# Kernel tuning notes

Hardware: AMD Instinct MI355X
Metric: run time of the kernel (lower is better)

Reference implementation:

```python
import jax, jax.numpy as jnp
import numpy as np

N = 20000      # nodes
E = 320000     # directed edges (self-loops added inside reference)
DIN = 128      # input_dim
HID = 64       # hidden_dim
H = 4          # num_heads
B = 16         # graphs in batch
OUT = 1        # output_dim
NEG_SLOPE = 0.2


def setup_inputs() -> dict:
    key = jax.random.key(0)
    ks = jax.random.split(key, 20)
    p = lambda k, shape: (jax.random.normal(k, shape, jnp.float32) * 0.05)
    x = jax.random.normal(ks[0], (N, DIN), jnp.float32)
    edge_index = jax.random.randint(ks[1], (2, E), 0, N, dtype=jnp.int64)
    batch = jnp.sort(jax.random.randint(ks[2], (N,), 0, B, dtype=jnp.int64))
    return {
        "x": x, "edge_index": edge_index, "batch": batch,
        # gat1: DIN -> (H, HID), concat
        "W1": p(ks[3], (DIN, H * HID)), "as1": p(ks[4], (H, HID)), "ad1": p(ks[5], (H, HID)), "b1": jnp.zeros((H * HID,), jnp.float32),
        # gat2: H*HID -> (H, HID), concat
        "W2": p(ks[6], (H * HID, H * HID)), "as2": p(ks[7], (H, HID)), "ad2": p(ks[8], (H, HID)), "b2": jnp.zeros((H * HID,), jnp.float32),
        # gat_out: H*HID -> (1, HID), mean (concat=False)
        "W3": p(ks[9], (H * HID, HID)), "as3": p(ks[10], (1, HID)), "ad3": p(ks[11], (1, HID)), "b3": jnp.zeros((HID,), jnp.float32),
        "wp": p(ks[12], (HID, 1)), "bp": jnp.zeros((1,), jnp.float32),
        "wr": p(ks[13], (HID, OUT)), "br": jnp.zeros((OUT,), jnp.float32),
    }


def _gat_layer(x, W, a_src, a_dst, bias, src, dst, heads, concat):
    n = x.shape[0]
    h = (x @ W).reshape(n, heads, -1)                      # [N,H,C]
    e_src = (h * a_src).sum(-1)                            # [N,H]
    e_dst = (h * a_dst).sum(-1)                            # [N,H]
    e = jax.nn.leaky_relu(e_src[src] + e_dst[dst], NEG_SLOPE)  # [Etot,H]
    # segment softmax over destination node (self-loops guarantee non-empty)
    m = jax.ops.segment_max(e, dst, num_segments=n)
    e = jnp.exp(e - m[dst])
    den = jax.ops.segment_sum(e, dst, num_segments=n)
    alpha = e / den[dst]                                   # [Etot,H]
    out = jax.ops.segment_sum(h[src] * alpha[..., None], dst, num_segments=n)  # [N,H,C]
    out = out.reshape(n, -1) if concat else out.mean(axis=1)
    return out + bias


def reference(x, edge_index, batch, W1, as1, ad1, b1, W2, as2, ad2, b2,
              W3, as3, ad3, b3, wp, bp, wr, br):
    n = x.shape[0]
    loops = jnp.arange(n, dtype=edge_index.dtype)
    src = jnp.concatenate([edge_index[0], loops])
    dst = jnp.concatenate([edge_index[1], loops])

    h = jax.nn.elu(_gat_layer(x, W1, as1, ad1, b1, src, dst, H, True))
    h = jax.nn.elu(_gat_layer(h, W2, as2, ad2, b2, src, dst, H, True))
    h = jax.nn.elu(_gat_layer(h, W3, as3, ad3, b3, src, dst, 1, False))  # [N,HID]

    attn = jax.nn.sigmoid(h @ wp + bp)                     # [N,1]
    hw = h * attn                                          # [N,HID]
    sums = jax.ops.segment_sum(hw, batch, num_segments=B)  # [B,HID]
    counts = jax.ops.segment_sum(jnp.ones((n,), hw.dtype), batch, num_segments=B)
    pooled = sums / jnp.maximum(counts, 1.0)[:, None]
    return pooled @ wr + br                                # [B,OUT]
```

## Files before the change

kernel.cpp:

```cpp
#include <hip/hip_runtime.h>


typedef unsigned short u16;
typedef __attribute__((ext_vector_type(8))) short bf16x8;
typedef __attribute__((ext_vector_type(4))) float f32x4;

__device__ __forceinline__ u16 bf16rn(float x) {
    unsigned u = __float_as_uint(x);
    u += 0x7FFFu + ((u >> 16) & 1u);
    return (u16)(u >> 16);
}
__device__ __forceinline__ float bf16f(u16 h) {
    return __uint_as_float(((unsigned)h) << 16);
}

__device__ __forceinline__ void gload16(const u16* g, u16* l) {
    __builtin_amdgcn_global_load_lds(
        (const __attribute__((address_space(1))) unsigned int*)g,
        (__attribute__((address_space(3))) unsigned int*)l, 16, 0, 0);
}

__global__ void edge_hist_k(const int* __restrict__ ei, int E, int n, int* __restrict__ deg) {
    int i = blockIdx.x * blockDim.x + threadIdx.x;
    if (i >= E + n) return;
    int dst = (i < E) ? ei[E + i] : (i - E);
    atomicAdd(&deg[dst], 1);
}

__global__ __launch_bounds__(1024) void scan_excl_k(const int* __restrict__ deg, int* __restrict__ rowptr,
                                                    int* __restrict__ cursor, int n) {
    __shared__ int part[1024];
    int tid = threadIdx.x;
    int chunk = (n + 1023) / 1024;
    int lo = tid * chunk;
    int hi = lo + chunk;
    if (lo > n) lo = n;
    if (hi > n) hi = n;
    int s = 0;
    for (int i = lo; i < hi; ++i) s += deg[i];
    part[tid] = s;
    __syncthreads();
    for (int off = 1; off < 1024; off <<= 1) {
        int v = (tid >= off) ? part[tid - off] : 0;
        __syncthreads();
        part[tid] += v;
        __syncthreads();
    }
    int run = (tid == 0) ? 0 : part[tid - 1];
    for (int i = lo; i < hi; ++i) {
        rowptr[i] = run;
        cursor[i] = run;
        run += deg[i];
    }
    if (tid == 1023) rowptr[n] = run;
}

__global__ void edge_scatter_k(const int* __restrict__ ei, int E, int n,
                               int* __restrict__ cursor, int* __restrict__ srcs) {
    int i = blockIdx.x * blockDim.x + threadIdx.x;
    if (i >= E + n) return;
    int src, dst;
    if (i < E) { src = ei[i]; dst = ei[E + i]; }
    else       { src = i - E; dst = src; }
    int pos = atomicAdd(&cursor[dst], 1);
    srcs[pos] = src;
}

__global__ void split_bf16_k(const float* __restrict__ in, u16* __restrict__ hi,
                             u16* __restrict__ lo, int n4) {
    int i = blockIdx.x * 256 + threadIdx.x;
    if (i >= n4) return;
    float4 v = reinterpret_cast<const float4*>(in)[i];
    u16 hx = bf16rn(v.x), hy = bf16rn(v.y), hz = bf16rn(v.z), hw = bf16rn(v.w);
    ushort4 H = make_ushort4(hx, hy, hz, hw);
    ushort4 L = make_ushort4(bf16rn(v.x - bf16f(hx)), bf16rn(v.y - bf16f(hy)),
                             bf16rn(v.z - bf16f(hz)), bf16rn(v.w - bf16f(hw)));
    reinterpret_cast<ushort4*>(hi)[i] = H;
    reinterpret_cast<ushort4*>(lo)[i] = L;
}

__global__ void splitT_bf16_k(const float* __restrict__ W, u16* __restrict__ thi,
                              u16* __restrict__ tlo, int K, int Nn) {
    int idx = blockIdx.x * 256 + threadIdx.x;
    if (idx >= K * Nn) return;
    int k = idx / Nn, nn = idx - k * Nn;
    float v = W[idx];
    u16 h = bf16rn(v);
    u16 l = bf16rn(v - bf16f(h));
    thi[(size_t)nn * K + k] = h;
    tlo[(size_t)nn * K + k] = l;
}

template <int NF>
__global__ __launch_bounds__(256) void gemm_lds_k(
        const u16* __restrict__ Ahi, const u16* __restrict__ Alo,
        const u16* __restrict__ Bthi, const u16* __restrict__ Btlo,
        float* __restrict__ C, int M, int Nn, int K) {
    __shared__ u16 Ah[2][4][64 * 8];
    __shared__ u16 Al[2][4][64 * 8];
    const int mb = (M + 63) >> 6;
    const int mi = blockIdx.x % mb;
    const int ni = blockIdx.x / mb;
    const int m0 = mi * 64;
    const int n0 = ni * (NF * 64);
    const int wv = threadIdx.x >> 6;
    const int lane = threadIdx.x & 63;
    const int rr = lane & 15;
    const int kg = lane >> 4;

    int srow = m0 + lane; if (srow > M - 1) srow = M - 1;
    const u16* sh = Ahi + (size_t)srow * K + wv * 8;
    const u16* sl = Alo + (size_t)srow * K + wv * 8;

    const u16* pbh[NF];
    const u16* pbl[NF];
#pragma unroll
    for (int nf = 0; nf < NF; ++nf) {
        int col = n0 + (wv * NF + nf) * 16 + rr;
        pbh[nf] = Bthi + (size_t)col * K + kg * 8;
        pbl[nf] = Btlo + (size_t)col * K + kg * 8;
    }

    f32x4 acc[4][NF];
#pragma unroll
    for (int mf = 0; mf < 4; ++mf)
#pragma unroll
        for (int nf = 0; nf < NF; ++nf) acc[mf][nf] = (f32x4){0.f, 0.f, 0.f, 0.f};

    bf16x8 bhc[NF], blc[NF], bhn[NF], bln[NF];
#pragma unroll
    for (int nf = 0; nf < NF; ++nf) {
        bhc[nf] = *reinterpret_cast<const bf16x8*>(pbh[nf]);
        blc[nf] = *reinterpret_cast<const bf16x8*>(pbl[nf]);
    }
    gload16(sh, &Ah[0][wv][0]);
    gload16(sl, &Al[0][wv][0]);
    __syncthreads();

    const int NT = K >> 5;
    for (int t = 0; t < NT; ++t) {
        const int cur = t & 1;
        if (t + 1 < NT) {
            const int kc = (t + 1) << 5;
#pragma unroll
            for (int nf = 0; nf < NF; ++nf) {
                bhn[nf] = *reinterpret_cast<const bf16x8*>(pbh[nf] + kc);
                bln[nf] = *reinterpret_cast<const bf16x8*>(pbl[nf] + kc);
            }
            gload16(sh + kc, &Ah[cur ^ 1][wv][0]);
            gload16(sl + kc, &Al[cur ^ 1][wv][0]);
        }
        bf16x8 ah[4], al[4];
#pragma unroll
        for (int mf = 0; mf < 4; ++mf) {
            ah[mf] = *reinterpret_cast<const bf16x8*>(&Ah[cur][kg][(mf * 16 + rr) * 8]);
            al[mf] = *reinterpret_cast<const bf16x8*>(&Al[cur][kg][(mf * 16 + rr) * 8]);
        }
#pragma unroll
        for (int mf = 0; mf < 4; ++mf)
#pragma unroll
            for (int nf = 0; nf < NF; ++nf) {
                acc[mf][nf] = __builtin_amdgcn_mfma_f32_16x16x32_bf16(ah[mf], bhc[nf], acc[mf][nf], 0, 0, 0);
                acc[mf][nf] = __builtin_amdgcn_mfma_f32_16x16x32_bf16(ah[mf], blc[nf], acc[mf][nf], 0, 0, 0);
                acc[mf][nf] = __builtin_amdgcn_mfma_f32_16x16x32_bf16(al[mf], bhc[nf], acc[mf][nf], 0, 0, 0);
            }
#pragma unroll
        for (int nf = 0; nf < NF; ++nf) { bhc[nf] = bhn[nf]; blc[nf] = bln[nf]; }
        __syncthreads();
    }

#pragma unroll
    for (int mf = 0; mf < 4; ++mf)
#pragma unroll
        for (int nf = 0; nf < NF; ++nf)
#pragma unroll
            for (int rg = 0; rg < 4; ++rg) {
                int row = m0 + mf * 16 + kg * 4 + rg;
                if (row < M)
                    C[(size_t)row * Nn + n0 + (wv * NF + nf) * 16 + rr] = acc[mf][nf][rg];
            }
}

__global__ void attn_scores4_k(const float* __restrict__ hin, const float* __restrict__ a_src,
                               const float* __restrict__ a_dst, float* __restrict__ esrc,
                               float* __restrict__ edst, int n) {
    int node = blockIdx.x * 4 + (threadIdx.x >> 6);
    int lane = threadIdx.x & 63;
    if (node >= n) return;
    float4 hv  = *reinterpret_cast<const float4*>(&hin[(size_t)node * 256 + lane * 4]);
    float4 asv = *reinterpret_cast<const float4*>(&a_src[lane * 4]);
    float4 adv = *reinterpret_cast<const float4*>(&a_dst[lane * 4]);
    float vs = hv.x * asv.x + hv.y * asv.y + hv.z * asv.z + hv.w * asv.w;
    float vd = hv.x * adv.x + hv.y * adv.y + hv.z * adv.z + hv.w * adv.w;
#pragma unroll
    for (int off = 8; off; off >>= 1) {
        vs += __shfl_xor(vs, off);
        vd += __shfl_xor(vd, off);
    }
    if ((lane & 15) == 0) {
        int h = lane >> 4;
        esrc[node * 4 + h] = vs;
        edst[node * 4 + h] = vd;
    }
}

__global__ void attn_scores1_k(const float* __restrict__ hin, const float* __restrict__ a_src,
                               const float* __restrict__ a_dst, float* __restrict__ esrc,
                               float* __restrict__ edst, int n) {
    int node = blockIdx.x * 4 + (threadIdx.x >> 6);
    int lane = threadIdx.x & 63;
    if (node >= n) return;
    float hv = hin[(size_t)node * 64 + lane];
    float vs = hv * a_src[lane];
    float vd = hv * a_dst[lane];
#pragma unroll
    for (int off = 32; off; off >>= 1) {
        vs += __shfl_xor(vs, off);
        vd += __shfl_xor(vd, off);
    }
    if (lane == 0) { esrc[node] = vs; edst[node] = vd; }
}

__global__ __launch_bounds__(256) void gat_aggregate4_k(
        const float* __restrict__ hin, const float* __restrict__ esrc,
        const float* __restrict__ edst, const int* __restrict__ rowptr,
        const int* __restrict__ srcs, const float* __restrict__ bias,
        u16* __restrict__ ghi, u16* __restrict__ glo, int n) {
    int d = blockIdx.x * 4 + (threadIdx.x >> 6);
    int lane = threadIdx.x & 63;
    if (d >= n) return;
    int hh = lane >> 4;
    float ed = edst[d * 4 + hh];
    int lo = rowptr[d], hi = rowptr[d + 1];
    float4 acc = make_float4(0.f, 0.f, 0.f, 0.f);
    float den = 0.f;
    for (int base = lo; base < hi; base += 64) {
        int cnt = min(64, hi - base);
        int sv = (lane < cnt) ? srcs[base + lane] : 0;
        int s0 = __shfl(sv, 0);
        float es0 = esrc[s0 * 4 + hh];
        float4 h0 = *reinterpret_cast<const float4*>(&hin[(size_t)s0 * 256 + lane * 4]);
        float es1 = 0.f;
        float4 h1 = h0;
        if (cnt > 1) {
            int s1 = __shfl(sv, 1);
            es1 = esrc[s1 * 4 + hh];
            h1 = *reinterpret_cast<const float4*>(&hin[(size_t)s1 * 256 + lane * 4]);
        }
        for (int j = 0; j < cnt; ++j) {
            float es = es0;
            float4 hv = h0;
            es0 = es1; h0 = h1;
            if (j + 2 < cnt) {
                int s2 = __shfl(sv, j + 2);
                es1 = esrc[s2 * 4 + hh];
                h1 = *reinterpret_cast<const float4*>(&hin[(size_t)s2 * 256 + lane * 4]);
            }
            float e = es + ed;
            e = (e >= 0.f) ? e : 0.2f * e;
            float w = __expf(e);
            den += w;
            acc.x = fmaf(w, hv.x, acc.x);
            acc.y = fmaf(w, hv.y, acc.y);
            acc.z = fmaf(w, hv.z, acc.z);
            acc.w = fmaf(w, hv.w, acc.w);
        }
    }
    float inv = 1.f / den;
    float4 bv = *reinterpret_cast<const float4*>(&bias[lane * 4]);
    float4 o;
    o.x = acc.x * inv + bv.x;
    o.y = acc.y * inv + bv.y;
    o.z = acc.z * inv + bv.z;
    o.w = acc.w * inv + bv.w;
    o.x = (o.x > 0.f) ? o.x : expm1f(o.x);
    o.y = (o.y > 0.f) ? o.y : expm1f(o.y);
    o.z = (o.z > 0.f) ? o.z : expm1f(o.z);
    o.w = (o.w > 0.f) ? o.w : expm1f(o.w);
    u16 hx = bf16rn(o.x), hy = bf16rn(o.y), hz = bf16rn(o.z), hw = bf16rn(o.w);
    ushort4 H = make_ushort4(hx, hy, hz, hw);
    ushort4 L = make_ushort4(bf16rn(o.x - bf16f(hx)), bf16rn(o.y - bf16f(hy)),
                             bf16rn(o.z - bf16f(hz)), bf16rn(o.w - bf16f(hw)));
    *reinterpret_cast<ushort4*>(&ghi[(size_t)d * 256 + lane * 4]) = H;
    *reinterpret_cast<ushort4*>(&glo[(size_t)d * 256 + lane * 4]) = L;
}

__global__ __launch_bounds__(256) void gat_aggregate1_attn_k(
        const float* __restrict__ hin, const float* __restrict__ esrc,
        const float* __restrict__ edst, const int* __restrict__ rowptr,
        const int* __restrict__ srcs, const float* __restrict__ bias,
        const float* __restrict__ wp, const float* __restrict__ bp,
        float* __restrict__ gout, float* __restrict__ attn, int n) {
    int d = blockIdx.x * 4 + (threadIdx.x >> 6);
    int lane = threadIdx.x & 63;
    if (d >= n) return;
    float ed = edst[d];
    int lo = rowptr[d], hi = rowptr[d + 1];
    float den = 0.f, acc = 0.f;
    for (int base = lo; base < hi; base += 64) {
        int cnt = min(64, hi - base);
        int sv = (lane < cnt) ? srcs[base + lane] : 0;
        int s0 = __shfl(sv, 0);
        float es_nxt = esrc[s0];
        float h_nxt = hin[(size_t)s0 * 64 + lane];
        for (int j = 0; j < cnt; ++j) {
            float es = es_nxt;
            float hv = h_nxt;
            if (j + 1 < cnt) {
                int s1 = __shfl(sv, j + 1);
                es_nxt = esrc[s1];
                h_nxt = hin[(size_t)s1 * 64 + lane];
            }
            float e = es + ed;
            e = (e >= 0.f) ? e : 0.2f * e;
            float w = __expf(e);
            den += w;
            acc = fmaf(w, hv, acc);
        }
    }
    float o = acc / den + bias[lane];
    o = (o > 0.f) ? o : expm1f(o);
    gout[(size_t)d * 64 + lane] = o;
    float v = o * wp[lane];
#pragma unroll
    for (int off = 32; off; off >>= 1) v += __shfl_xor(v, off);
    if (lane == 0) attn[d] = 1.f / (1.f + __expf(-(v + bp[0])));
}

__global__ void pool_partial_k(const float* __restrict__ g3, const float* __restrict__ attn,
                               const int* __restrict__ batch, int n, float* __restrict__ sums) {
    int wid = blockIdx.x * (blockDim.x >> 6) + (threadIdx.x >> 6);
    int lane = threadIdx.x & 63;
    int nwaves = gridDim.x * (blockDim.x >> 6);
    int per = (n + nwaves - 1) / nwaves;
    int i0 = wid * per;
    int i1 = i0 + per;
    if (i1 > n) i1 = n;
    if (i0 >= i1) return;
    int cur = batch[i0];
    float acc = 0.f;
    for (int i = i0; i < i1; ++i) {
        int b = batch[i];
        if (b != cur) {
            atomicAdd(&sums[cur * 64 + lane], acc);
            acc = 0.f;
            cur = b;
        }
        acc += g3[(size_t)i * 64 + lane] * attn[i];
    }
    atomicAdd(&sums[cur * 64 + lane], acc);
}

__global__ void regress_k(const float* __restrict__ sums, const int* __restrict__ batch, int n,
                          const float* __restrict__ wr, const float* __restrict__ br,
                          float* __restrict__ out, int B) {
    int b = threadIdx.x >> 6;
    int lane = threadIdx.x & 63;
    if (b >= B) return;
    int lo = 0, hi = n;
    while (lo < hi) { int mid = (lo + hi) >> 1; if (batch[mid] < b) lo = mid + 1; else hi = mid; }
    int seg_lo = lo;
    lo = 0; hi = n;
    while (lo < hi) { int mid = (lo + hi) >> 1; if (batch[mid] < b + 1) lo = mid + 1; else hi = mid; }
    float cnt = (float)(lo - seg_lo);
    if (cnt < 1.f) cnt = 1.f;
    float v = (sums[b * 64 + lane] / cnt) * wr[lane];
#pragma unroll
    for (int off = 32; off; off >>= 1) v += __shfl_xor(v, off);
    if (lane == 0) out[b] = v + br[0];
}

extern "C" void kernel_launch(void* const* d_in, const int* in_sizes, int n_in,
                              void* d_out, int out_size, void* d_ws, size_t ws_size,
                              hipStream_t stream) {
    const float* x   = (const float*)d_in[0];
    const int*   ei  = (const int*)d_in[1];
    const int*   bat = (const int*)d_in[2];
    const float* W1  = (const float*)d_in[3];
    const float* as1 = (const float*)d_in[4];
    const float* ad1 = (const float*)d_in[5];
    const float* b1  = (const float*)d_in[6];
    const float* W2  = (const float*)d_in[7];
    const float* as2 = (const float*)d_in[8];
    const float* ad2 = (const float*)d_in[9];
    const float* b2  = (const float*)d_in[10];
    const float* W3  = (const float*)d_in[11];
    const float* as3 = (const float*)d_in[12];
    const float* ad3 = (const float*)d_in[13];
    const float* b3  = (const float*)d_in[14];
    const float* wp  = (const float*)d_in[15];
    const float* bp  = (const float*)d_in[16];
    const float* wr  = (const float*)d_in[17];
    const float* br  = (const float*)d_in[18];
    float* out = (float*)d_out;

    const int N    = in_sizes[2];
    const int E    = in_sizes[1] / 2;
    const int DIN  = in_sizes[0] / N;
    const int Etot = E + N;
    const int Bc   = out_size;

    char* ws = (char*)d_ws;
    size_t off = 0;
    auto alloc = [&](size_t bytes) {
        void* p = ws + off;
        off = (off + bytes + 255) & ~(size_t)255;
        return p;
    };
    int*   deg    = (int*)alloc((size_t)N * 4);
    int*   rowptr = (int*)alloc((size_t)(N + 1) * 4);
    int*   cursor = (int*)alloc((size_t)N * 4);
    int*   srcs   = (int*)alloc((size_t)Etot * 4);
    float* bufA   = (float*)alloc((size_t)N * 256 * 4);
    u16*   Ahi    = (u16*)alloc((size_t)N * 256 * 2);
    u16*   Alo    = (u16*)alloc((size_t)N * 256 * 2);
    float* h3     = (float*)alloc((size_t)N * 64 * 4);
    float* g3     = (float*)alloc((size_t)N * 64 * 4);
    float* esrc   = (float*)alloc((size_t)N * 4 * 4);
    float* edst   = (float*)alloc((size_t)N * 4 * 4);
    float* attn   = (float*)alloc((size_t)N * 4);
    float* sums   = (float*)alloc((size_t)Bc * 64 * 4);
    u16*   w1hi   = (u16*)alloc((size_t)256 * DIN * 2);
    u16*   w1lo   = (u16*)alloc((size_t)256 * DIN * 2);
    u16*   w2hi   = (u16*)alloc((size_t)256 * 256 * 2);
    u16*   w2lo   = (u16*)alloc((size_t)256 * 256 * 2);
    u16*   w3hi   = (u16*)alloc((size_t)64 * 256 * 2);
    u16*   w3lo   = (u16*)alloc((size_t)64 * 256 * 2);
    (void)ws_size;

    hipMemsetAsync(deg, 0, (size_t)N * 4, stream);
    int eb = (Etot + 255) / 256;
    edge_hist_k<<<eb, 256, 0, stream>>>(ei, E, N, deg);
    scan_excl_k<<<1, 1024, 0, stream>>>(deg, rowptr, cursor, N);
    edge_scatter_k<<<eb, 256, 0, stream>>>(ei, E, N, cursor, srcs);

    splitT_bf16_k<<<(DIN * 256 + 255) / 256, 256, 0, stream>>>(W1, w1hi, w1lo, DIN, 256);
    splitT_bf16_k<<<(256 * 256 + 255) / 256, 256, 0, stream>>>(W2, w2hi, w2lo, 256, 256);
    splitT_bf16_k<<<(256 * 64 + 255) / 256, 256, 0, stream>>>(W3, w3hi, w3lo, 256, 64);
    split_bf16_k<<<(N * DIN / 4 + 255) / 256, 256, 0, stream>>>(x, Ahi, Alo, N * DIN / 4);

    const int mb = (N + 63) / 64;
    int nb4 = (N + 3) / 4;

    gemm_lds_k<2><<<mb * 2, 256, 0, stream>>>(Ahi, Alo, w1hi, w1lo, bufA, N, 256, DIN);
    attn_scores4_k<<<nb4, 256, 0, stream>>>(bufA, as1, ad1, esrc, edst, N);
    gat_aggregate4_k<<<nb4, 256, 0, stream>>>(bufA, esrc, edst, rowptr, srcs, b1, Ahi, Alo, N);

    gemm_lds_k<2><<<mb * 2, 256, 0, stream>>>(Ahi, Alo, w2hi, w2lo, bufA, N, 256, 256);
    attn_scores4_k<<<nb4, 256, 0, stream>>>(bufA, as2, ad2, esrc, edst, N);
    gat_aggregate4_k<<<nb4, 256, 0, stream>>>(bufA, esrc, edst, rowptr, srcs, b2, Ahi, Alo, N);

    gemm_lds_k<1><<<mb, 256, 0, stream>>>(Ahi, Alo, w3hi, w3lo, h3, N, 64, 256);
    attn_scores1_k<<<nb4, 256, 0, stream>>>(h3, as3, ad3, esrc, edst, N);
    gat_aggregate1_attn_k<<<nb4, 256, 0, stream>>>(h3, esrc, edst, rowptr, srcs, b3, wp, bp, g3, attn, N);

    hipMemsetAsync(sums, 0, (size_t)Bc * 64 * 4, stream);
    pool_partial_k<<<256, 256, 0, stream>>>(g3, attn, bat, N, sums);
    regress_k<<<1, 1024, 0, stream>>>(sums, bat, N, wr, br, out, Bc);
}
```

Measured before the change: 298.2 us.

## Parallelize edge-weight computation across lanes and deepen gather prefetch in aggregation kernels

The edge attention logits and exponentials are now computed in parallel across wave lanes, one edge per lane, and reduced with shuffles. Previously each wave did this serially per edge, with a dependent esrc load each time. The weighted feature accumulation then broadcasts weights via shuffles and prefetches four neighbor rows at a time to raise memory-level parallelism. Tail edges are clamped and given zero weight, which adds extra shuffles and some redundant loads on short rows.

```diff
diff --git a/kernel.cpp b/kernel.cpp
--- a/kernel.cpp
+++ b/kernel.cpp
@@ -229,41 +229,51 @@
     int d = blockIdx.x * 4 + (threadIdx.x >> 6);
     int lane = threadIdx.x & 63;
     if (d >= n) return;
-    int hh = lane >> 4;
+    const int hh = lane >> 4;
+    const int jj = lane & 15;
     float ed = edst[d * 4 + hh];
     int lo = rowptr[d], hi = rowptr[d + 1];
     float4 acc = make_float4(0.f, 0.f, 0.f, 0.f);
     float den = 0.f;
-    for (int base = lo; base < hi; base += 64) {
-        int cnt = min(64, hi - base);
-        int sv = (lane < cnt) ? srcs[base + lane] : 0;
-        int s0 = __shfl(sv, 0);
-        float es0 = esrc[s0 * 4 + hh];
-        float4 h0 = *reinterpret_cast<const float4*>(&hin[(size_t)s0 * 256 + lane * 4]);
-        float es1 = 0.f;
-        float4 h1 = h0;
-        if (cnt > 1) {
-            int s1 = __shfl(sv, 1);
-            es1 = esrc[s1 * 4 + hh];
-            h1 = *reinterpret_cast<const float4*>(&hin[(size_t)s1 * 256 + lane * 4]);
-        }
-        for (int j = 0; j < cnt; ++j) {
-            float es = es0;
-            float4 hv = h0;
-            es0 = es1; h0 = h1;
-            if (j + 2 < cnt) {
-                int s2 = __shfl(sv, j + 2);
-                es1 = esrc[s2 * 4 + hh];
-                h1 = *reinterpret_cast<const float4*>(&hin[(size_t)s2 * 256 + lane * 4]);
-            }
-            float e = es + ed;
-            e = (e >= 0.f) ? e : 0.2f * e;
-            float w = __expf(e);
-            den += w;
-            acc.x = fmaf(w, hv.x, acc.x);
-            acc.y = fmaf(w, hv.y, acc.y);
-            acc.z = fmaf(w, hv.z, acc.z);
-            acc.w = fmaf(w, hv.w, acc.w);
+    for (int base = lo; base < hi; base += 32) {
+        int cnt = min(32, hi - base);
+        int i0 = base + jj, i1 = base + 16 + jj;
+        int s0 = srcs[(i0 < hi) ? i0 : lo];
+        int s1 = srcs[(i1 < hi) ? i1 : lo];
+        float e0 = esrc[s0 * 4 + hh] + ed;
+        e0 = (e0 >= 0.f) ? e0 : 0.2f * e0;
+        float w0 = (jj < cnt) ? __expf(e0) : 0.f;
+        float e1 = esrc[s1 * 4 + hh] + ed;
+        e1 = (e1 >= 0.f) ? e1 : 0.2f * e1;
+        float w1 = (jj + 16 < cnt) ? __expf(e1) : 0.f;
+        float ws = w0 + w1;
+#pragma unroll
+        for (int off = 1; off < 16; off <<= 1) ws += __shfl_xor(ws, off);
+        den += ws;
+        auto loadrow = [&](int j) -> float4 {
+            j = (j < cnt) ? j : (cnt - 1);
+            int sp = __shfl((j < 16) ? s0 : s1, j & 15);
+            return *reinterpret_cast<const float4*>(&hin[(size_t)sp * 256 + lane * 4]);
+        };
+        auto wsel = [&](int j) -> float {
+            return __shfl((j < 16) ? w0 : w1, (lane & 48) | (j & 15));
+        };
+        float4 p0 = loadrow(0), p1 = loadrow(1), p2 = loadrow(2), p3 = loadrow(3);
+        for (int j = 0; j < cnt; j += 4) {
+            float4 q0 = p0, q1 = p1, q2 = p2, q3 = p3;
+            p0 = loadrow(j + 4);
+            p1 = loadrow(j + 5);
+            p2 = loadrow(j + 6);
+            p3 = loadrow(j + 7);
+            float wA = wsel(j), wB = wsel(j + 1), wC = wsel(j + 2), wD = wsel(j + 3);
+            acc.x = fmaf(wA, q0.x, acc.x); acc.y = fmaf(wA, q0.y, acc.y);
+            acc.z = fmaf(wA, q0.z, acc.z); acc.w = fmaf(wA, q0.w, acc.w);
+            acc.x = fmaf(wB, q1.x, acc.x); acc.y = fmaf(wB, q1.y, acc.y);
+            acc.z = fmaf(wB, q1.z, acc.z); acc.w = fmaf(wB, q1.w, acc.w);
+            acc.x = fmaf(wC, q2.x, acc.x); acc.y = fmaf(wC, q2.y, acc.y);
+            acc.z = fmaf(wC, q2.z, acc.z); acc.w = fmaf(wC, q2.w, acc.w);
+            acc.x = fmaf(wD, q3.x, acc.x); acc.y = fmaf(wD, q3.y, acc.y);
+            acc.z = fmaf(wD, q3.z, acc.z); acc.w = fmaf(wD, q3.w, acc.w);
         }
     }
     float inv = 1.f / den;
@@ -299,23 +309,31 @@
     float den = 0.f, acc = 0.f;
     for (int base = lo; base < hi; base += 64) {
         int cnt = min(64, hi - base);
-        int sv = (lane < cnt) ? srcs[base + lane] : 0;
-        int s0 = __shfl(sv, 0);
-        float es_nxt = esrc[s0];
-        float h_nxt = hin[(size_t)s0 * 64 + lane];
-        for (int j = 0; j < cnt; ++j) {
-            float es = es_nxt;
-            float hv = h_nxt;
-            if (j + 1 < cnt) {
-                int s1 = __shfl(sv, j + 1);
-                es_nxt = esrc[s1];
-                h_nxt = hin[(size_t)s1 * 64 + lane];
-            }
-            float e = es + ed;
-            e = (e >= 0.f) ? e : 0.2f * e;
-            float w = __expf(e);
-            den += w;
-            acc = fmaf(w, hv, acc);
+        int idx = base + lane;
+        int s = srcs[(idx < hi) ? idx : lo];
+        float e = esrc[s] + ed;
+        e = (e >= 0.f) ? e : 0.2f * e;
+        float w = (lane < cnt) ? __expf(e) : 0.f;
+        float ws = w;
+#pragma unroll
+        for (int off = 1; off < 64; off <<= 1) ws += __shfl_xor(ws, off);
+        den += ws;
+        auto loadrow = [&](int j) -> float {
+            j = (j < cnt) ? j : (cnt - 1);
+            int sp = __shfl(s, j);
+            return hin[(size_t)sp * 64 + lane];
+        };
+        float p0 = loadrow(0), p1 = loadrow(1), p2 = loadrow(2), p3 = loadrow(3);
+        for (int j = 0; j < cnt; j += 4) {
+            float q0 = p0, q1 = p1, q2 = p2, q3 = p3;
+            p0 = loadrow(j + 4);
+            p1 = loadrow(j + 5);
+            p2 = loadrow(j + 6);
+            p3 = loadrow(j + 7);
+            acc = fmaf(__shfl(w, j), q0, acc);
+            acc = fmaf(__shfl(w, j + 1), q1, acc);
+            acc = fmaf(__shfl(w, j + 2), q2, acc);
+            acc = fmaf(__shfl(w, j + 3), q3, acc);
         }
     }
     float o = acc / den + bias[lane];
```

Measured after the change: 281.5 us. 5.6% less time.
